# Kernel tuning notes

Hardware: AMD Instinct MI355X
Metric: run time of the kernel (lower is better)

Reference implementation:

```python
import jax, jax.numpy as jnp
import numpy as np

NUM_HEADS = 16
HEAD_DIM = 64
MAX_POS = 2048  # max_position_embeddings


def setup_inputs() -> dict:
    key = jax.random.key(0)
    ks = jax.random.split(key, 8)
    B, S, H = 4, 1024, 1024
    s = 1.0 / np.sqrt(H)
    return {
        "hidden_states": jax.random.normal(ks[0], (B, S, H), jnp.float32),
        "attention_mask": jnp.zeros((B, 1, 1, S), jnp.float32),
        "Wq": jax.random.normal(ks[1], (H, H), jnp.float32) * s,
        "bq": jnp.zeros((H,), jnp.float32),
        "Wk": jax.random.normal(ks[2], (H, H), jnp.float32) * s,
        "bk": jnp.zeros((H,), jnp.float32),
        "Wv": jax.random.normal(ks[3], (H, H), jnp.float32) * s,
        "bv": jnp.zeros((H,), jnp.float32),
        "dist_emb": jax.random.normal(ks[4], (2 * MAX_POS - 1, HEAD_DIM), jnp.float32) * 0.02,
    }


def _split_heads(x):
    B, S, _ = x.shape
    return x.reshape(B, S, NUM_HEADS, HEAD_DIM).transpose(0, 2, 1, 3)  # [B,H,S,dh]


def reference(hidden_states, attention_mask, Wq, bq, Wk, bk, Wv, bv, dist_emb):
    B, S, _ = hidden_states.shape
    q = _split_heads(hidden_states @ Wq + bq)
    k = _split_heads(hidden_states @ Wk + bk)
    v = _split_heads(hidden_states @ Wv + bv)

    scores = jnp.einsum("bhld,bhrd->bhlr", q, k)

    # relative_key_query positional bias
    pos = jnp.arange(S)
    distance = pos[:, None] - pos[None, :]                 # [S,S]
    pe = dist_emb[distance + MAX_POS - 1]                   # [S,S,dh]
    scores = scores + jnp.einsum("bhld,lrd->bhlr", q, pe)
    scores = scores + jnp.einsum("bhrd,lrd->bhlr", k, pe)

    scores = scores / np.sqrt(HEAD_DIM).astype(np.float32)
    scores = scores + attention_mask                        # additive mask broadcast
    probs = jax.nn.softmax(scores, axis=-1)                 # dropout is identity in eval

    ctx = jnp.einsum("bhlr,bhrd->bhld", probs, v)
    ctx = ctx.transpose(0, 2, 1, 3).reshape(B, S, NUM_HEADS * HEAD_DIM)
    return ctx
```

## Files before the change

kernel.cpp:

```cpp
#include <hip/hip_runtime.h>
#include <hip/hip_bf16.h>

typedef __hip_bfloat16 bf16;
typedef __attribute__((ext_vector_type(8))) short bf16x8;
typedef __attribute__((ext_vector_type(4))) float f32x4;

#define MFMA(a, b, c) __builtin_amdgcn_mfma_f32_16x16x32_bf16((a), (b), (c), 0, 0, 0)
#define DPPF(x, ctrl) __builtin_bit_cast(float, __builtin_amdgcn_update_dpp(0, __builtin_bit_cast(int, (x)), (ctrl), 0xF, 0xF, true))

static __device__ __forceinline__ float red16max(float x) {
    x = fmaxf(x, DPPF(x, 0xB1));
    x = fmaxf(x, DPPF(x, 0x4E));
    x = fmaxf(x, DPPF(x, 0x124));
    x = fmaxf(x, DPPF(x, 0x128));
    return x;
}
static __device__ __forceinline__ float red16sum(float x) {
    x += DPPF(x, 0xB1);
    x += DPPF(x, 0x4E);
    x += DPPF(x, 0x124);
    x += DPPF(x, 0x128);
    return x;
}
static __device__ __forceinline__ unsigned short f2bu(float x) {
    __hip_bfloat16 h = __float2bfloat16(x);
    return *reinterpret_cast<unsigned short*>(&h);
}

__global__ void prep_convert(const float* __restrict__ X, const float* __restrict__ DE,
                             bf16* __restrict__ Xb, bf16* __restrict__ DEb) {
    int i = blockIdx.x * blockDim.x + threadIdx.x;
    if (i < 1048576) {
        float4 v = reinterpret_cast<const float4*>(X)[i];
        bf16* d = Xb + 4 * i;
        d[0] = __float2bfloat16(v.x); d[1] = __float2bfloat16(v.y);
        d[2] = __float2bfloat16(v.z); d[3] = __float2bfloat16(v.w);
    } else {
        int j = i - 1048576;
        if (j < 65520) {
            float4 v = reinterpret_cast<const float4*>(DE)[j];
            bf16* d = DEb + 4 * j;
            d[0] = __float2bfloat16(v.x); d[1] = __float2bfloat16(v.y);
            d[2] = __float2bfloat16(v.z); d[3] = __float2bfloat16(v.w);
        }
    }
}

__global__ void prep_transpose_w(const float* __restrict__ Wq, const float* __restrict__ Wk,
                                 const float* __restrict__ Wv, bf16* __restrict__ WTb) {
    const float* W = (blockIdx.z == 0) ? Wq : (blockIdx.z == 1) ? Wk : Wv;
    bf16* WT = WTb + (size_t)blockIdx.z * (1024u * 1024u);
    __shared__ float t[64][65];
    int tid = threadIdx.x;
    int col = tid & 63;
    int r4 = tid >> 6;
    int i0 = blockIdx.x * 64, o0 = blockIdx.y * 64;
    for (int it = 0; it < 16; ++it) {
        int row = it * 4 + r4;
        t[row][col] = W[(size_t)(i0 + row) * 1024 + o0 + col];
    }
    __syncthreads();
    for (int it = 0; it < 16; ++it) {
        int row = it * 4 + r4;
        WT[(size_t)(o0 + row) * 1024 + i0 + col] = __float2bfloat16(t[col][row]);
    }
}

__global__ __launch_bounds__(256, 2) void proj_gemm(
    const bf16* __restrict__ Xb, const bf16* __restrict__ WTb,
    const float* __restrict__ bq, const float* __restrict__ bk, const float* __restrict__ bv,
    bf16* __restrict__ Qb, bf16* __restrict__ Kb, bf16* __restrict__ VTb) {
    int proj = blockIdx.z;
    const bf16* W = WTb + (size_t)proj * (1024u * 1024u);
    const float* bias = (proj == 0) ? bq : (proj == 1) ? bk : bv;

    __shared__ bf16 XT[128][72];
    __shared__ bf16 WTt[128][72];

    int tid = threadIdx.x;
    int w = tid >> 6, lane = tid & 63, g = lane >> 4, li = lane & 15;
    int wr = w >> 1, wc = w & 1;
    int m0 = blockIdx.x * 128, n0 = blockIdx.y * 128;

    f32x4 acc[4][4];
    for (int mt = 0; mt < 4; mt++)
        for (int nt = 0; nt < 4; nt++) acc[mt][nt] = {0.f, 0.f, 0.f, 0.f};

    for (int ks = 0; ks < 16; ++ks) {
        for (int it = 0; it < 4; ++it) {
            int idx = tid + 256 * it;
            int row = idx >> 3, c = (idx & 7) * 8;
            *reinterpret_cast<bf16x8*>(&XT[row][c]) =
                *reinterpret_cast<const bf16x8*>(Xb + (size_t)(m0 + row) * 1024 + ks * 64 + c);
            *reinterpret_cast<bf16x8*>(&WTt[row][c]) =
                *reinterpret_cast<const bf16x8*>(W + (size_t)(n0 + row) * 1024 + ks * 64 + c);
        }
        __syncthreads();
        for (int kk = 0; kk < 2; ++kk) {
            bf16x8 af[4], bfr[4];
            for (int mt = 0; mt < 4; mt++)
                af[mt] = *reinterpret_cast<const bf16x8*>(&XT[64 * wr + 16 * mt + li][32 * kk + 8 * g]);
            for (int nt = 0; nt < 4; nt++)
                bfr[nt] = *reinterpret_cast<const bf16x8*>(&WTt[64 * wc + 16 * nt + li][32 * kk + 8 * g]);
            for (int mt = 0; mt < 4; mt++)
                for (int nt = 0; nt < 4; nt++)
                    acc[mt][nt] = MFMA(af[mt], bfr[nt], acc[mt][nt]);
        }
        __syncthreads();
    }

    for (int mt = 0; mt < 4; mt++)
        for (int nt = 0; nt < 4; nt++) {
            int n = n0 + 64 * wc + 16 * nt + li;
            int h = n >> 6, d = n & 63;
            float bv_ = bias[n];
            for (int r = 0; r < 4; r++) {
                int m = m0 + 64 * wr + 16 * mt + 4 * g + r;
                int b = m >> 10, s = m & 1023;
                bf16 o = __float2bfloat16(acc[mt][nt][r] + bv_);
                if (proj == 0)      Qb[((size_t)(b * 16 + h) * 1024 + s) * 64 + d] = o;
                else if (proj == 1) Kb[((size_t)(b * 16 + h) * 1024 + s) * 64 + d] = o;
                else                VTb[((size_t)(b * 16 + h) * 64 + d) * 1024 + s] = o;
            }
        }
}

__global__ __launch_bounds__(256, 2) void attn_fused(
    const bf16* __restrict__ Qg, const bf16* __restrict__ Kg,
    const bf16* __restrict__ VTg, const bf16* __restrict__ DEb,
    const float* __restrict__ mask, float* __restrict__ out) {
    const int S = 1024, D = 64;
    int p = blockIdx.x;
    int bh = (p & 7) * 8 + ((p >> 3) >> 4);
    int qb = (p >> 3) & 15;
    int b = bh >> 4;
    int L0 = qb * 64;

    int tid = threadIdx.x;
    int w = tid >> 6, lane = tid & 63, g = lane >> 4, li = lane & 15;

    __shared__ bf16 K_lds[64][72];
    __shared__ bf16 VT_lds[2][64][72];
    __shared__ bf16 DE_lds[128][72];
    __shared__ bf16 QD_T[4][80][20];
    __shared__ bf16 KD_T[80][68];
    __shared__ bf16 P_lds[4][16][72];

    const bf16* Qh = Qg + (size_t)bh * S * D;
    const bf16* Kh = Kg + (size_t)bh * S * D;
    const bf16* Vh = VTg + (size_t)bh * D * S;
    const float* maskb = mask + b * S;

    int srow = tid >> 3;
    int scol = (tid & 7) * 8;

    bf16x8 qa0, qa1;
    {
        const bf16* qrow = Qh + (size_t)(L0 + 16 * w + li) * D;
        qa0 = *reinterpret_cast<const bf16x8*>(qrow + 8 * g);
        qa1 = *reinterpret_cast<const bf16x8*>(qrow + 32 + 8 * g);
    }

    const char* qdb = (const char*)(&QD_T[w][0][0]) + (40 * (4 * g - li + 15) + 8 * g);
    const char* kdb = (const char*)(&KD_T[0][0]) + (136 * (16 * w + 4 * g - li + 15) + 2 * li);

    int de00 = L0 + 1984;
    {
        for (int c = 0; c < 2; ++c) {
            int row = srow + 32 * c;
            *reinterpret_cast<bf16x8*>(&K_lds[row][scol]) =
                *reinterpret_cast<const bf16x8*>(Kh + (size_t)row * D + scol);
            *reinterpret_cast<bf16x8*>(&VT_lds[0][row][scol]) =
                *reinterpret_cast<const bf16x8*>(Vh + (size_t)row * S + scol);
        }
        for (int c = 0; c < 4; ++c) {
            int j = srow + 32 * c;
            *reinterpret_cast<bf16x8*>(&DE_lds[(de00 + j) & 127][scol]) =
                *reinterpret_cast<const bf16x8*>(DEb + (size_t)(de00 + j) * 64 + scol);
        }
    }

    f32x4 acc_o[4];
    for (int dt = 0; dt < 4; dt++) acc_o[dt] = {0.f, 0.f, 0.f, 0.f};
    float m_run[4], l_run[4];
    for (int r = 0; r < 4; r++) { m_run[r] = -1e30f; l_run[r] = 0.f; }

    __syncthreads();

    for (int kt = 0; kt < 16; ++kt) {
        int r0 = kt * 64;
        int de0 = de00 - r0;
        bool has_next = (kt < 15);

        bf16x8 sK0, sK1, sV0, sV1, sD0, sD1;
        if (has_next) {
            int r0n = r0 + 64;
            int dlo = de0 - 64;
            sK0 = *reinterpret_cast<const bf16x8*>(Kh + (size_t)(r0n + srow) * D + scol);
            sK1 = *reinterpret_cast<const bf16x8*>(Kh + (size_t)(r0n + srow + 32) * D + scol);
            sV0 = *reinterpret_cast<const bf16x8*>(Vh + (size_t)srow * S + r0n + scol);
            sV1 = *reinterpret_cast<const bf16x8*>(Vh + (size_t)(srow + 32) * S + r0n + scol);
            sD0 = *reinterpret_cast<const bf16x8*>(DEb + (size_t)(dlo + srow) * 64 + scol);
            sD1 = *reinterpret_cast<const bf16x8*>(DEb + (size_t)(dlo + srow + 32) * 64 + scol);
        }

        f32x4 s_acc[4];
        __builtin_amdgcn_s_setprio(1);
        for (int nt = 0; nt < 4; ++nt) {
            bf16x8 kb0 = *reinterpret_cast<const bf16x8*>(&K_lds[16 * nt + li][8 * g]);
            bf16x8 kb1 = *reinterpret_cast<const bf16x8*>(&K_lds[16 * nt + li][32 + 8 * g]);
            f32x4 a = {0.f, 0.f, 0.f, 0.f};
            a = MFMA(qa0, kb0, a);
            a = MFMA(qa1, kb1, a);
            s_acc[nt] = a;
        }
        {
            int kr = 16 * (3 - w) + li;
            bf16x8 ka0 = *reinterpret_cast<const bf16x8*>(&K_lds[kr][8 * g]);
            bf16x8 ka1 = *reinterpret_cast<const bf16x8*>(&K_lds[kr][32 + 8 * g]);
            for (int jt = 0; jt < 5; ++jt) {
                int dr = (de0 + 16 * w + 16 * jt + li) & 127;
                bf16x8 d0 = *reinterpret_cast<const bf16x8*>(&DE_lds[dr][8 * g]);
                bf16x8 d1 = *reinterpret_cast<const bf16x8*>(&DE_lds[dr][32 + 8 * g]);
                f32x4 aq = {0.f, 0.f, 0.f, 0.f};
                aq = MFMA(qa0, d0, aq);
                aq = MFMA(qa1, d1, aq);
                f32x4 ak = {0.f, 0.f, 0.f, 0.f};
                ak = MFMA(ka0, d0, ak);
                ak = MFMA(ka1, d1, ak);
                ushort4 uq;
                uq.x = f2bu(aq[0]); uq.y = f2bu(aq[1]); uq.z = f2bu(aq[2]); uq.w = f2bu(aq[3]);
                *reinterpret_cast<ushort4*>(&QD_T[w][16 * jt + li][4 * g]) = uq;
                ushort4 uk;
                uk.x = f2bu(ak[0]); uk.y = f2bu(ak[1]); uk.z = f2bu(ak[2]); uk.w = f2bu(ak[3]);
                *reinterpret_cast<ushort4*>(&KD_T[16 * jt + li][16 * (3 - w) + 4 * g]) = uk;
            }
        }
        __builtin_amdgcn_s_setprio(0);
        __syncthreads();

        float qdv[4][4], kdv[4][4];
        for (int nt = 0; nt < 4; ++nt)
            for (int r = 0; r < 4; ++r) {
                qdv[nt][r] = __bfloat162float(*(const __hip_bfloat16*)(qdb + 42 * r + 640 * (3 - nt)));
                kdv[nt][r] = __bfloat162float(*(const __hip_bfloat16*)(kdb + 136 * r + 32 * nt));
            }

        float pr[4][4];
        float tm[4] = {-1e30f, -1e30f, -1e30f, -1e30f};
        for (int nt = 0; nt < 4; ++nt) {
            float mk = maskb[r0 + 16 * nt + li];
            for (int r = 0; r < 4; ++r) {
                float sv = (s_acc[nt][r] + qdv[nt][r] + kdv[nt][r]) * 0.125f + mk;
                pr[nt][r] = sv;
                tm[r] = fmaxf(tm[r], sv);
            }
        }
        for (int r = 0; r < 4; ++r) tm[r] = red16max(tm[r]);
        int skip = (tm[0] <= m_run[0]) & (tm[1] <= m_run[1]) &
                   (tm[2] <= m_run[2]) & (tm[3] <= m_run[3]);
        bool all_skip = __all(skip);
        for (int r = 0; r < 4; ++r) {
            float mnew, scl;
            if (all_skip) { mnew = m_run[r]; }
            else {
                mnew = fmaxf(m_run[r], tm[r]);
                scl = exp2f((m_run[r] - mnew) * 1.44269504f);
                m_run[r] = mnew;
            }
            float ssum = 0.f;
            for (int nt = 0; nt < 4; ++nt) {
                float pv = exp2f((pr[nt][r] - mnew) * 1.44269504f);
                pr[nt][r] = pv;
                ssum += pv;
            }
            ssum = red16sum(ssum);
            if (all_skip) l_run[r] += ssum;
            else {
                l_run[r] = l_run[r] * scl + ssum;
                for (int dt = 0; dt < 4; dt++) acc_o[dt][r] *= scl;
            }
        }

        for (int nt = 0; nt < 4; nt++)
            for (int r = 0; r < 4; r++)
                P_lds[w][4 * g + r][16 * nt + li] = __float2bfloat16(pr[nt][r]);
        bf16x8 pa0 = *reinterpret_cast<const bf16x8*>(&P_lds[w][li][8 * g]);
        bf16x8 pa1 = *reinterpret_cast<const bf16x8*>(&P_lds[w][li][32 + 8 * g]);
        __builtin_amdgcn_s_setprio(1);
        for (int dt = 0; dt < 4; dt++) {
            bf16x8 vb0 = *reinterpret_cast<const bf16x8*>(&VT_lds[kt & 1][16 * dt + li][8 * g]);
            bf16x8 vb1 = *reinterpret_cast<const bf16x8*>(&VT_lds[kt & 1][16 * dt + li][32 + 8 * g]);
            acc_o[dt] = MFMA(pa0, vb0, acc_o[dt]);
            acc_o[dt] = MFMA(pa1, vb1, acc_o[dt]);
        }
        __builtin_amdgcn_s_setprio(0);

        if (has_next) {
            int dlo = de0 - 64;
            *reinterpret_cast<bf16x8*>(&K_lds[srow][scol]) = sK0;
            *reinterpret_cast<bf16x8*>(&K_lds[srow + 32][scol]) = sK1;
            *reinterpret_cast<bf16x8*>(&VT_lds[(kt + 1) & 1][srow][scol]) = sV0;
            *reinterpret_cast<bf16x8*>(&VT_lds[(kt + 1) & 1][srow + 32][scol]) = sV1;
            *reinterpret_cast<bf16x8*>(&DE_lds[(dlo + srow) & 127][scol]) = sD0;
            *reinterpret_cast<bf16x8*>(&DE_lds[(dlo + srow + 32) & 127][scol]) = sD1;
        }
        __syncthreads();
    }

    int h = bh & 15;
    for (int dt = 0; dt < 4; dt++)
        for (int r = 0; r < 4; r++) {
            int srow_ = L0 + 16 * w + 4 * g + r;
            out[((size_t)b * 1024 + srow_) * 1024 + (size_t)h * 64 + 16 * dt + li] =
                acc_o[dt][r] / l_run[r];
        }
}

extern "C" void kernel_launch(void* const* d_in, const int* in_sizes, int n_in,
                              void* d_out, int out_size, void* d_ws, size_t ws_size,
                              hipStream_t stream) {
    const float* X   = (const float*)d_in[0];
    const float* msk = (const float*)d_in[1];
    const float* Wq  = (const float*)d_in[2];
    const float* bq  = (const float*)d_in[3];
    const float* Wk  = (const float*)d_in[4];
    const float* bk  = (const float*)d_in[5];
    const float* Wv  = (const float*)d_in[6];
    const float* bv  = (const float*)d_in[7];
    const float* DE  = (const float*)d_in[8];
    float* out = (float*)d_out;

    bf16* ws  = (bf16*)d_ws;
    bf16* Xb  = ws;
    bf16* WTb = ws + 4194304;
    bf16* DEb = ws + 7340032;
    bf16* Qb  = ws + 7602176;
    bf16* Kb  = ws + 11796480;
    bf16* VTb = ws + 15990784;

    prep_convert<<<4352, 256, 0, stream>>>(X, DE, Xb, DEb);
    prep_transpose_w<<<dim3(16, 16, 3), 256, 0, stream>>>(Wq, Wk, Wv, WTb);
    proj_gemm<<<dim3(32, 8, 3), 256, 0, stream>>>(Xb, WTb, bq, bk, bv, Qb, Kb, VTb);
    attn_fused<<<dim3(1024), 256, 0, stream>>>(Qb, Kb, VTb, DEb, msk, out);
}
```

Before: 156.0 us.

## Transpose MFMA operand order so each lane owns one query row in attention

Swaps the A/B operands of every MFMA so the score and output accumulators are transposed, letting each lane hold a single query row. Row max and sum now need two cross-quad shuffles instead of four-step DPP reductions over four rows, and the running m/l state becomes scalar. Shared memory is merged into one manually laid-out buffer, bias tiles are written as packed bf16 pairs, and the scale is folded into the exp2 constant. The output is staged through LDS so global stores become coalesced float4 writes. This carries a risk of address-arithmetic errors in the hand-computed LDS offsets.

```diff
diff --git a/kernel.cpp b/kernel.cpp
--- a/kernel.cpp
+++ b/kernel.cpp
@@ -4,27 +4,29 @@
 typedef __hip_bfloat16 bf16;
 typedef __attribute__((ext_vector_type(8))) short bf16x8;
 typedef __attribute__((ext_vector_type(4))) float f32x4;
+typedef __attribute__((ext_vector_type(2))) unsigned int u32x2;
 
 #define MFMA(a, b, c) __builtin_amdgcn_mfma_f32_16x16x32_bf16((a), (b), (c), 0, 0, 0)
-#define DPPF(x, ctrl) __builtin_bit_cast(float, __builtin_amdgcn_update_dpp(0, __builtin_bit_cast(int, (x)), (ctrl), 0xF, 0xF, true))
-
-static __device__ __forceinline__ float red16max(float x) {
-    x = fmaxf(x, DPPF(x, 0xB1));
-    x = fmaxf(x, DPPF(x, 0x4E));
-    x = fmaxf(x, DPPF(x, 0x124));
-    x = fmaxf(x, DPPF(x, 0x128));
+
+static __device__ __forceinline__ float bf2f(bf16 b) { return __bfloat162float(b); }
+
+static __device__ __forceinline__ unsigned pk2(float a, float b) {
+    bf16 ha = __float2bfloat16(a);
+    bf16 hb = __float2bfloat16(b);
+    unsigned short ua = *reinterpret_cast<unsigned short*>(&ha);
+    unsigned short ub = *reinterpret_cast<unsigned short*>(&hb);
+    return (unsigned)ua | ((unsigned)ub << 16);
+}
+
+static __device__ __forceinline__ float quad_max(float x) {
+    x = fmaxf(x, __shfl_xor(x, 16));
+    x = fmaxf(x, __shfl_xor(x, 32));
     return x;
 }
-static __device__ __forceinline__ float red16sum(float x) {
-    x += DPPF(x, 0xB1);
-    x += DPPF(x, 0x4E);
-    x += DPPF(x, 0x124);
-    x += DPPF(x, 0x128);
+static __device__ __forceinline__ float quad_sum(float x) {
+    x += __shfl_xor(x, 16);
+    x += __shfl_xor(x, 32);
     return x;
-}
-static __device__ __forceinline__ unsigned short f2bu(float x) {
-    __hip_bfloat16 h = __float2bfloat16(x);
-    return *reinterpret_cast<unsigned short*>(&h);
 }
 
 __global__ void prep_convert(const float* __restrict__ X, const float* __restrict__ DE,
@@ -130,26 +132,25 @@
     const bf16* __restrict__ VTg, const bf16* __restrict__ DEb,
     const float* __restrict__ mask, float* __restrict__ out) {
     const int S = 1024, D = 64;
-    int p = blockIdx.x;
-    int bh = (p & 7) * 8 + ((p >> 3) >> 4);
-    int qb = (p >> 3) & 15;
-    int b = bh >> 4;
+    const float C8 = 0.18033688011112042f;
+    int p_ = blockIdx.x;
+    int bh = (p_ & 7) * 8 + ((p_ >> 3) >> 4);
+    int qb = (p_ >> 3) & 15;
+    int b = bh >> 4, h = bh & 15;
     int L0 = qb * 64;
 
     int tid = threadIdx.x;
     int w = tid >> 6, lane = tid & 63, g = lane >> 4, li = lane & 15;
 
-    __shared__ bf16 K_lds[64][72];
-    __shared__ bf16 VT_lds[2][64][72];
-    __shared__ bf16 DE_lds[128][72];
-    __shared__ bf16 QD_T[4][80][20];
-    __shared__ bf16 KD_T[80][68];
-    __shared__ bf16 P_lds[4][16][72];
+    __shared__ __align__(16) char smem[77824];
+    bf16 (*K_lds)[72]      = reinterpret_cast<bf16(*)[72]>(smem);
+    bf16 (*VT_lds)[64][72] = reinterpret_cast<bf16(*)[64][72]>(smem + 9216);
+    bf16 (*DE_lds)[72]     = reinterpret_cast<bf16(*)[72]>(smem + 27648);
 
     const bf16* Qh = Qg + (size_t)bh * S * D;
     const bf16* Kh = Kg + (size_t)bh * S * D;
     const bf16* Vh = VTg + (size_t)bh * D * S;
-    const float* maskb = mask + b * S;
+    const float* mrow = mask + (size_t)b * S + 4 * g;
 
     int srow = tid >> 3;
     int scol = (tid & 7) * 8;
@@ -161,8 +162,11 @@
         qa1 = *reinterpret_cast<const bf16x8*>(qrow + 32 + 8 * g);
     }
 
-    const char* qdb = (const char*)(&QD_T[w][0][0]) + (40 * (4 * g - li + 15) + 8 * g);
-    const char* kdb = (const char*)(&KD_T[0][0]) + (136 * (16 * w + 4 * g - li + 15) + 2 * li);
+    const char* qdb = smem + 46080 + 2816 * w + 178 * li - 8 * g;
+    const char* kdb = smem + 57344 + 696 * g + 32 * w + 2 * li + 30;
+    char* qsp = smem + 46080 + 2816 * w + 176 * li + 8 * g;
+    char* ksp = smem + 57344 + 176 * (48 - 16 * w + li) + 8 * g;
+    char* Pp = smem + 68608 + 2304 * w + 144 * li;
 
     int de00 = L0 + 1984;
     {
@@ -182,8 +186,7 @@
 
     f32x4 acc_o[4];
     for (int dt = 0; dt < 4; dt++) acc_o[dt] = {0.f, 0.f, 0.f, 0.f};
-    float m_run[4], l_run[4];
-    for (int r = 0; r < 4; r++) { m_run[r] = -1e30f; l_run[r] = 0.f; }
+    float m_run = -1e30f, l_run = 0.f;
 
     __syncthreads();
 
@@ -204,95 +207,99 @@
             sD1 = *reinterpret_cast<const bf16x8*>(DEb + (size_t)(dlo + srow + 32) * 64 + scol);
         }
 
+        __builtin_amdgcn_s_setprio(1);
         f32x4 s_acc[4];
-        __builtin_amdgcn_s_setprio(1);
+        #pragma unroll
         for (int nt = 0; nt < 4; ++nt) {
             bf16x8 kb0 = *reinterpret_cast<const bf16x8*>(&K_lds[16 * nt + li][8 * g]);
             bf16x8 kb1 = *reinterpret_cast<const bf16x8*>(&K_lds[16 * nt + li][32 + 8 * g]);
-            f32x4 a = {0.f, 0.f, 0.f, 0.f};
-            a = MFMA(qa0, kb0, a);
-            a = MFMA(qa1, kb1, a);
-            s_acc[nt] = a;
+            f32x4 z = {0.f, 0.f, 0.f, 0.f};
+            z = MFMA(kb0, qa0, z);
+            z = MFMA(kb1, qa1, z);
+            s_acc[nt] = z;
         }
         {
             int kr = 16 * (3 - w) + li;
             bf16x8 ka0 = *reinterpret_cast<const bf16x8*>(&K_lds[kr][8 * g]);
             bf16x8 ka1 = *reinterpret_cast<const bf16x8*>(&K_lds[kr][32 + 8 * g]);
+            #pragma unroll
             for (int jt = 0; jt < 5; ++jt) {
                 int dr = (de0 + 16 * w + 16 * jt + li) & 127;
                 bf16x8 d0 = *reinterpret_cast<const bf16x8*>(&DE_lds[dr][8 * g]);
                 bf16x8 d1 = *reinterpret_cast<const bf16x8*>(&DE_lds[dr][32 + 8 * g]);
                 f32x4 aq = {0.f, 0.f, 0.f, 0.f};
-                aq = MFMA(qa0, d0, aq);
-                aq = MFMA(qa1, d1, aq);
+                aq = MFMA(d0, qa0, aq);
+                aq = MFMA(d1, qa1, aq);
                 f32x4 ak = {0.f, 0.f, 0.f, 0.f};
-                ak = MFMA(ka0, d0, ak);
-                ak = MFMA(ka1, d1, ak);
-                ushort4 uq;
-                uq.x = f2bu(aq[0]); uq.y = f2bu(aq[1]); uq.z = f2bu(aq[2]); uq.w = f2bu(aq[3]);
-                *reinterpret_cast<ushort4*>(&QD_T[w][16 * jt + li][4 * g]) = uq;
-                ushort4 uk;
-                uk.x = f2bu(ak[0]); uk.y = f2bu(ak[1]); uk.z = f2bu(ak[2]); uk.w = f2bu(ak[3]);
-                *reinterpret_cast<ushort4*>(&KD_T[16 * jt + li][16 * (3 - w) + 4 * g]) = uk;
+                ak = MFMA(d0, ka0, ak);
+                ak = MFMA(d1, ka1, ak);
+                u32x2 uq = {pk2(aq[0], aq[1]), pk2(aq[2], aq[3])};
+                *reinterpret_cast<u32x2*>(qsp + 32 * jt) = uq;
+                u32x2 uk = {pk2(ak[0], ak[1]), pk2(ak[2], ak[3])};
+                *reinterpret_cast<u32x2*>(ksp + 32 * jt) = uk;
             }
         }
         __builtin_amdgcn_s_setprio(0);
         __syncthreads();
 
-        float qdv[4][4], kdv[4][4];
+        float u[4][4];
+        float lmax = -1e30f;
+        #pragma unroll
+        for (int nt = 0; nt < 4; ++nt) {
+            #pragma unroll
+            for (int r = 0; r < 4; ++r) {
+                float qd = bf2f(*reinterpret_cast<const bf16*>(qdb + (126 - 32 * nt - 2 * r)));
+                float kd = bf2f(*reinterpret_cast<const bf16*>(kdb + (2816 * nt + 174 * r)));
+                float mk = mrow[r0 + 16 * nt + r];
+                float uu = s_acc[nt][r] + qd + kd;
+                uu = __builtin_fmaf(mk, 8.0f, uu);
+                u[nt][r] = uu;
+                lmax = fmaxf(lmax, uu);
+            }
+        }
+        float tm = quad_max(lmax);
+        bool noskip = !__all(tm <= m_run);
+        float scl = 1.0f;
+        if (noskip) {
+            float mnew = fmaxf(m_run, tm);
+            scl = exp2f((m_run - mnew) * C8);
+            m_run = mnew;
+        }
+        float nmc = -m_run * C8;
+        float pv[4][4];
+        #pragma unroll
         for (int nt = 0; nt < 4; ++nt)
-            for (int r = 0; r < 4; ++r) {
-                qdv[nt][r] = __bfloat162float(*(const __hip_bfloat16*)(qdb + 42 * r + 640 * (3 - nt)));
-                kdv[nt][r] = __bfloat162float(*(const __hip_bfloat16*)(kdb + 136 * r + 32 * nt));
-            }
-
-        float pr[4][4];
-        float tm[4] = {-1e30f, -1e30f, -1e30f, -1e30f};
+            #pragma unroll
+            for (int r = 0; r < 4; ++r)
+                pv[nt][r] = exp2f(__builtin_fmaf(u[nt][r], C8, nmc));
+        float t0 = (pv[0][0] + pv[0][1]) + (pv[0][2] + pv[0][3]);
+        float t1 = (pv[1][0] + pv[1][1]) + (pv[1][2] + pv[1][3]);
+        float t2 = (pv[2][0] + pv[2][1]) + (pv[2][2] + pv[2][3]);
+        float t3 = (pv[3][0] + pv[3][1]) + (pv[3][2] + pv[3][3]);
+        float qs = quad_sum((t0 + t1) + (t2 + t3));
+        if (noskip) {
+            l_run = l_run * scl + qs;
+            #pragma unroll
+            for (int dt = 0; dt < 4; dt++) acc_o[dt] *= scl;
+        } else {
+            l_run += qs;
+        }
+
+        #pragma unroll
         for (int nt = 0; nt < 4; ++nt) {
-            float mk = maskb[r0 + 16 * nt + li];
-            for (int r = 0; r < 4; ++r) {
-                float sv = (s_acc[nt][r] + qdv[nt][r] + kdv[nt][r]) * 0.125f + mk;
-                pr[nt][r] = sv;
-                tm[r] = fmaxf(tm[r], sv);
-            }
-        }
-        for (int r = 0; r < 4; ++r) tm[r] = red16max(tm[r]);
-        int skip = (tm[0] <= m_run[0]) & (tm[1] <= m_run[1]) &
-                   (tm[2] <= m_run[2]) & (tm[3] <= m_run[3]);
-        bool all_skip = __all(skip);
-        for (int r = 0; r < 4; ++r) {
-            float mnew, scl;
-            if (all_skip) { mnew = m_run[r]; }
-            else {
-                mnew = fmaxf(m_run[r], tm[r]);
-                scl = exp2f((m_run[r] - mnew) * 1.44269504f);
-                m_run[r] = mnew;
-            }
-            float ssum = 0.f;
-            for (int nt = 0; nt < 4; ++nt) {
-                float pv = exp2f((pr[nt][r] - mnew) * 1.44269504f);
-                pr[nt][r] = pv;
-                ssum += pv;
-            }
-            ssum = red16sum(ssum);
-            if (all_skip) l_run[r] += ssum;
-            else {
-                l_run[r] = l_run[r] * scl + ssum;
-                for (int dt = 0; dt < 4; dt++) acc_o[dt][r] *= scl;
-            }
-        }
-
-        for (int nt = 0; nt < 4; nt++)
-            for (int r = 0; r < 4; r++)
-                P_lds[w][4 * g + r][16 * nt + li] = __float2bfloat16(pr[nt][r]);
-        bf16x8 pa0 = *reinterpret_cast<const bf16x8*>(&P_lds[w][li][8 * g]);
-        bf16x8 pa1 = *reinterpret_cast<const bf16x8*>(&P_lds[w][li][32 + 8 * g]);
+            u32x2 pp = {pk2(pv[nt][0], pv[nt][1]), pk2(pv[nt][2], pv[nt][3])};
+            *reinterpret_cast<u32x2*>(Pp + 32 * nt + 8 * g) = pp;
+        }
+        bf16x8 pb0 = *reinterpret_cast<const bf16x8*>(Pp + 16 * g);
+        bf16x8 pb1 = *reinterpret_cast<const bf16x8*>(Pp + 64 + 16 * g);
+
         __builtin_amdgcn_s_setprio(1);
+        #pragma unroll
         for (int dt = 0; dt < 4; dt++) {
-            bf16x8 vb0 = *reinterpret_cast<const bf16x8*>(&VT_lds[kt & 1][16 * dt + li][8 * g]);
-            bf16x8 vb1 = *reinterpret_cast<const bf16x8*>(&VT_lds[kt & 1][16 * dt + li][32 + 8 * g]);
-            acc_o[dt] = MFMA(pa0, vb0, acc_o[dt]);
-            acc_o[dt] = MFMA(pa1, vb1, acc_o[dt]);
+            bf16x8 va0 = *reinterpret_cast<const bf16x8*>(&VT_lds[kt & 1][16 * dt + li][8 * g]);
+            bf16x8 va1 = *reinterpret_cast<const bf16x8*>(&VT_lds[kt & 1][16 * dt + li][32 + 8 * g]);
+            acc_o[dt] = MFMA(va0, pb0, acc_o[dt]);
+            acc_o[dt] = MFMA(va1, pb1, acc_o[dt]);
         }
         __builtin_amdgcn_s_setprio(0);
 
@@ -308,13 +315,22 @@
         __syncthreads();
     }
 
-    int h = bh & 15;
+    float inv = 1.0f / l_run;
+    float (*OT)[68] = reinterpret_cast<float (*)[68]>(smem + 27648);
+    #pragma unroll
     for (int dt = 0; dt < 4; dt++)
-        for (int r = 0; r < 4; r++) {
-            int srow_ = L0 + 16 * w + 4 * g + r;
-            out[((size_t)b * 1024 + srow_) * 1024 + (size_t)h * 64 + 16 * dt + li] =
-                acc_o[dt][r] / l_run[r];
-        }
+        #pragma unroll
+        for (int r = 0; r < 4; r++)
+            OT[16 * w + li][16 * dt + 4 * g + r] = acc_o[dt][r] * inv;
+    __syncthreads();
+    {
+        int q = tid >> 2, seg = tid & 3;
+        float* gout = out + ((size_t)(b * 1024 + L0 + q)) * 1024 + h * 64 + 16 * seg;
+        #pragma unroll
+        for (int j = 0; j < 4; ++j)
+            *reinterpret_cast<float4*>(gout + 4 * j) =
+                *reinterpret_cast<const float4*>(&OT[q][16 * seg + 4 * j]);
+    }
 }
 
 extern "C" void kernel_launch(void* const* d_in, const int* in_sizes, int n_in,
```

Result: slower. 164.2 us (+5.3%).
